# Kernel tuning notes

Measured on AMD Instinct MI355X. Metric: run time of the kernel, lower is better.

The kernel has to match this reference:

```python
import jax, jax.numpy as jnp
import numpy as np

B, N, F_IN, H, L = 4, 2048, 3, 32, 3
H2 = H // 2


def setup_inputs() -> dict:
    key = jax.random.key(0)
    ks = jax.random.split(key, 16)
    feats = jax.random.normal(ks[0], (B, N, F_IN), dtype=jnp.float32)
    coors = jax.random.normal(ks[1], (B, N, 3), dtype=jnp.float32) * 3.0
    adj = jax.random.randint(ks[2], (B, N, N), 0, 2).astype(bool)
    adj = adj | jnp.eye(N, dtype=bool)[None]  # self-loops so every row has a neighbor
    s = 0.1
    return {
        "feats": feats,
        "coors": coors,
        "adj_mat": adj,
        "W_in": jax.random.normal(ks[3], (F_IN, H), dtype=jnp.float32) * s,
        "Wq": jax.random.normal(ks[4], (L, H, H), dtype=jnp.float32) * s,
        "Wk": jax.random.normal(ks[5], (L, H, H), dtype=jnp.float32) * s,
        "Wv": jax.random.normal(ks[6], (L, H, H), dtype=jnp.float32) * s,
        "Wo": jax.random.normal(ks[7], (L, H, H), dtype=jnp.float32) * s,
        "W1": jax.random.normal(ks[8], (L, H, 2 * H), dtype=jnp.float32) * s,
        "W2": jax.random.normal(ks[9], (L, 2 * H, H), dtype=jnp.float32) * s,
        "coor_scale": jnp.full((L,), 0.1, dtype=jnp.float32),
        "Wf1": jax.random.normal(ks[10], (H, H2), dtype=jnp.float32) * s,
        "bf1": jnp.zeros((H2,), dtype=jnp.float32),
        "Wf2": jax.random.normal(ks[11], (H2, 3), dtype=jnp.float32) * s,
        "bf2": jnp.zeros((3,), dtype=jnp.float32),
    }


def _se3_forward(feats, coors, adj_mat, W_in, Wq, Wk, Wv, Wo, W1, W2, coor_scale):
    h = feats @ W_in                      # [B,N,H]
    x = coors
    neg = jnp.finfo(h.dtype).min
    inv_sqrt_d = 1.0 / jnp.sqrt(jnp.asarray(H, h.dtype))
    for l in range(L):                    # small static layer loop
        rel = x[:, :, None, :] - x[:, None, :, :]          # [B,N,N,3]
        dist2 = jnp.sum(rel * rel, axis=-1)                 # [B,N,N]
        q = h @ Wq[l]
        k = h @ Wk[l]
        v = h @ Wv[l]
        logits = jnp.einsum('bie,bje->bij', q, k) * inv_sqrt_d - dist2
        logits = jnp.where(adj_mat, logits, neg)
        attn = jax.nn.softmax(logits, axis=-1)              # [B,N,N]
        h = h + jnp.einsum('bij,bjd->bid', attn, v) @ Wo[l]
        # equivariant coordinate update (attention-weighted relative vectors)
        x = x + coor_scale[l] * jnp.einsum('bij,bijc->bic', attn, rel)
        h = h + jax.nn.relu(h @ W1[l]) @ W2[l]
    return h


def reference(feats, coors, adj_mat, W_in, Wq, Wk, Wv, Wo, W1, W2,
              coor_scale, Wf1, bf1, Wf2, bf2):
    h = _se3_forward(feats, coors, adj_mat, W_in, Wq, Wk, Wv, Wo, W1, W2, coor_scale)
    pooled = h.mean(axis=1)                                 # [B,H]
    out = jax.nn.relu(pooled @ Wf1 + bf1) @ Wf2 + bf2       # [B,3]
    return out
```

## Files before the change

### kernel.cpp

```cpp
#include <hip/hip_runtime.h>
#include <cstddef>
#include <cstdint>

#define N_     2048
#define H_     32
#define NEGF   (-1.0e30f)
#define LOG2E  1.4426950408889634f
#define C1F    (0.17677669529663687f * 1.4426950408889634f)
#define DEFER  16.0f
#define NCHUNK 8
#define CLEN   256
#define NRTOT  8192
#define PREC   20

#define AS1 __attribute__((address_space(1)))
#define AS3 __attribute__((address_space(3)))

typedef unsigned short ushortT;
typedef short v8s __attribute__((ext_vector_type(8)));
typedef float v4f __attribute__((ext_vector_type(4)));

__device__ __forceinline__ float exp2_fast(float x) {
    float r;
    asm("v_exp_f32 %0, %1" : "=v"(r) : "v"(x));
    return r;
}

__device__ __forceinline__ unsigned f2bf(float x) {
    unsigned u = __builtin_bit_cast(unsigned, x);
    return (u + 0x7FFFu + ((u >> 16) & 1u)) >> 16;
}

__global__ __launch_bounds__(256) void k_adjmask(const int* __restrict__ adj,
                                                 unsigned long long* __restrict__ mask) {
    size_t idx = (size_t)blockIdx.x * 256 + threadIdx.x;
    unsigned long long m = __ballot(adj[idx] != 0);
    if ((threadIdx.x & 63) == 0) mask[idx >> 6] = m;
}

__global__ __launch_bounds__(256) void k_init_qkv(const float* __restrict__ feats,
                                                  const float* __restrict__ W_in,
                                                  const float* __restrict__ Wq,
                                                  const float* __restrict__ Wk,
                                                  const float* __restrict__ Wv,
                                                  float* __restrict__ h,
                                                  ushortT* __restrict__ qb,
                                                  ushortT* __restrict__ kb,
                                                  ushortT* __restrict__ vb) {
    __shared__ float hs[8][33];
    int t = threadIdx.x;
    int rl = t >> 5, c = t & 31;
    int row = blockIdx.x * 8 + rl;
    float f0 = feats[row * 3 + 0], f1 = feats[row * 3 + 1], f2 = feats[row * 3 + 2];
    float hv = f0 * W_in[c] + f1 * W_in[32 + c] + f2 * W_in[64 + c];
    hs[rl][c] = hv;
    h[(row << 5) + c] = hv;
    __syncthreads();
    float aq = 0.f, ak = 0.f, av = 0.f;
#pragma unroll
    for (int d = 0; d < 32; ++d) {
        float hd = hs[rl][d];
        aq += hd * Wq[(d << 5) + c];
        ak += hd * Wk[(d << 5) + c];
        av += hd * Wv[(d << 5) + c];
    }
    qb[(row << 5) + c] = (ushortT)f2bf(aq * C1F);
    kb[(row << 5) + c] = (ushortT)f2bf(ak);
    vb[(row << 5) + c] = (ushortT)f2bf(av);
}

__global__ __launch_bounds__(256) void k_attn(const ushortT* __restrict__ qb,
                                              const ushortT* __restrict__ kb,
                                              const ushortT* __restrict__ vb,
                                              const float* __restrict__ xin,
                                              const unsigned long long* __restrict__ maskg,
                                              float* __restrict__ pm,
                                              float* __restrict__ ps,
                                              unsigned* __restrict__ pacc) {
    __shared__ __attribute__((aligned(16))) ushortT k_lds[2][64 * 32];
    __shared__ __attribute__((aligned(16))) ushortT vt_lds[2][32 * 72];
    __shared__ __attribute__((aligned(16))) float4  x_lds[2][64];
    __shared__ __attribute__((aligned(16))) ushortT p_lds[4][16 * 40];

    const int t = threadIdx.x;
    const int w = t >> 6, l = t & 63;
    const int g = l >> 4, q = l & 15;
    const int rowblk = blockIdx.x >> 3;
    const int cid    = blockIdx.x & 7;
    const int bN = (rowblk >> 5) << 11;
    const int j0 = cid << 8;
    const int rq = rowblk * 64 + w * 16 + q;

#define STAGE_TILE(BUF, TILE)                                                                  \
    do {                                                                                       \
        const int jj0 = (TILE) << 6;                                                           \
        __builtin_amdgcn_global_load_lds(                                                      \
            (const AS1 void*)((const char*)(kb + (((size_t)(bN + j0 + jj0)) << 5)) + t * 16),  \
            (AS3 void*)((char*)&k_lds[BUF][0] + t * 16), 16, 0, 0);                            \
        const int j_ = t & 63, grp_ = t >> 6;                                                  \
        const uint4 vv = *(const uint4*)(vb + (((size_t)(bN + j0 + jj0 + j_)) << 5) + grp_ * 8);\
        unsigned arr[4] = {vv.x, vv.y, vv.z, vv.w};                                            \
        _Pragma("unroll")                                                                      \
        for (int ii = 0; ii < 4; ++ii) {                                                       \
            vt_lds[BUF][(grp_ * 8 + 2 * ii) * 72 + j_]     = (ushortT)(arr[ii] & 0xffffu);     \
            vt_lds[BUF][(grp_ * 8 + 2 * ii + 1) * 72 + j_] = (ushortT)(arr[ii] >> 16);         \
        }                                                                                      \
        if (t < 64) {                                                                          \
            const float* xp_ = xin + ((size_t)(bN + j0 + jj0 + t)) * 3;                        \
            float4 xv_; xv_.x = xp_[0]; xv_.y = xp_[1]; xv_.z = xp_[2]; xv_.w = 0.f;           \
            x_lds[BUF][t] = xv_;                                                               \
        }                                                                                      \
    } while (0)

    const v8s qf = *(const v8s*)(qb + (((size_t)rq) << 5) + g * 8);
    const float xi0 = xin[rq * 3 + 0], xi1 = xin[rq * 3 + 1], xi2 = xin[rq * 3 + 2];

    v4f oA = {0.f, 0.f, 0.f, 0.f}, oB = {0.f, 0.f, 0.f, 0.f};
    float m = NEGF, sum = 0.f;
    float xa0 = 0.f, xa1 = 0.f, xa2 = 0.f;

    ushortT* pw = &p_lds[w][0];

    STAGE_TILE(0, 0);
    __syncthreads();

    int cur = 0;
#pragma unroll
    for (int tile = 0; tile < 4; ++tile) {
        if (tile < 3) STAGE_TILE(cur ^ 1, tile + 1);
        const unsigned long long mw = maskg[(((size_t)rq) << 5) + (cid << 2) + tile];

#pragma unroll
        for (int half = 0; half < 2; ++half) {
            const int jt = half * 32;
            v8s kA = *(const v8s*)(&k_lds[cur][0] + (jt + q) * 32 + g * 8);
            v8s kB = *(const v8s*)(&k_lds[cur][0] + (jt + 16 + q) * 32 + g * 8);
            v4f zero = {0.f, 0.f, 0.f, 0.f};
            v4f sA = __builtin_amdgcn_mfma_f32_16x16x32_bf16(kA, qf, zero, 0, 0, 0);
            v4f sB = __builtin_amdgcn_mfma_f32_16x16x32_bf16(kB, qf, zero, 0, 0, 0);

            float se[8];
            float4 xjA[4], xjB[4];
            float pot = NEGF;
#pragma unroll
            for (int reg = 0; reg < 4; ++reg) {
                const int jA = jt + 4 * g + reg, jB = jA + 16;
                xjA[reg] = x_lds[cur][jA];
                xjB[reg] = x_lds[cur][jB];
                float dA0 = xi0 - xjA[reg].x, dA1 = xi1 - xjA[reg].y, dA2 = xi2 - xjA[reg].z;
                float dB0 = xi0 - xjB[reg].x, dB1 = xi1 - xjB[reg].y, dB2 = xi2 - xjB[reg].z;
                float distA = fmaf(dA2, dA2, fmaf(dA1, dA1, dA0 * dA0));
                float distB = fmaf(dB2, dB2, fmaf(dB1, dB1, dB0 * dB0));
                const int bA = (int)((mw >> jA) & 1ULL);
                const int bB = (int)((mw >> jB) & 1ULL);
                se[reg]     = bA ? fmaf(distA, -LOG2E, sA[reg]) : NEGF;
                se[4 + reg] = bB ? fmaf(distB, -LOG2E, sB[reg]) : NEGF;
                pot = fmaxf(pot, fmaxf(se[reg], se[4 + reg]));
            }
            pot = fmaxf(pot, __shfl_xor(pot, 16));
            pot = fmaxf(pot, __shfl_xor(pot, 32));
            if (__any(pot - m > DEFER)) {
                float n2 = fmaxf(m, pot);
                float al = exp2_fast(m - n2);
                m = n2; sum *= al;
                v4f alv = {al, al, al, al};
                oA *= alv; oB *= alv;
                xa0 *= al; xa1 *= al; xa2 *= al;
            }
            float p[8];
#pragma unroll
            for (int i = 0; i < 8; ++i) { p[i] = exp2_fast(se[i] - m); sum += p[i]; }
#pragma unroll
            for (int reg = 0; reg < 4; ++reg) {
                xa0 = fmaf(p[reg], xjA[reg].x, fmaf(p[4 + reg], xjB[reg].x, xa0));
                xa1 = fmaf(p[reg], xjA[reg].y, fmaf(p[4 + reg], xjB[reg].y, xa1));
                xa2 = fmaf(p[reg], xjA[reg].z, fmaf(p[4 + reg], xjB[reg].z, xa2));
            }
            uint2 wA, wB;
            wA.x = f2bf(p[0]) | (f2bf(p[1]) << 16);
            wA.y = f2bf(p[2]) | (f2bf(p[3]) << 16);
            wB.x = f2bf(p[4]) | (f2bf(p[5]) << 16);
            wB.y = f2bf(p[6]) | (f2bf(p[7]) << 16);
            *(uint2*)(pw + q * 40 + 4 * g)      = wA;
            *(uint2*)(pw + q * 40 + 16 + 4 * g) = wB;
            v8s pf = *(const v8s*)(pw + q * 40 + 8 * g);
            v8s vA = *(const v8s*)(&vt_lds[cur][0] + q * 72 + jt + 8 * g);
            v8s vB = *(const v8s*)(&vt_lds[cur][0] + (16 + q) * 72 + jt + 8 * g);
            oA = __builtin_amdgcn_mfma_f32_16x16x32_bf16(vA, pf, oA, 0, 0, 0);
            oB = __builtin_amdgcn_mfma_f32_16x16x32_bf16(vB, pf, oB, 0, 0, 0);
        }
        __syncthreads();
        cur ^= 1;
    }
#undef STAGE_TILE

    sum += __shfl_xor(sum, 16); sum += __shfl_xor(sum, 32);
    xa0 += __shfl_xor(xa0, 16); xa0 += __shfl_xor(xa0, 32);
    xa1 += __shfl_xor(xa1, 16); xa1 += __shfl_xor(xa1, 32);
    xa2 += __shfl_xor(xa2, 16); xa2 += __shfl_xor(xa2, 32);

    unsigned* pb = pacc + ((size_t)cid * NRTOT + rq) * PREC;
    uint2 rA, rB;
    rA.x = f2bf(oA[0]) | (f2bf(oA[1]) << 16);
    rA.y = f2bf(oA[2]) | (f2bf(oA[3]) << 16);
    rB.x = f2bf(oB[0]) | (f2bf(oB[1]) << 16);
    rB.y = f2bf(oB[2]) | (f2bf(oB[3]) << 16);
    *(uint2*)(pb + 2 * g)     = rA;
    *(uint2*)(pb + 8 + 2 * g) = rB;
    if (g == 0) {
        float4 tl; tl.x = xa0; tl.y = xa1; tl.z = xa2; tl.w = 0.f;
        *(float4*)(pb + 16) = tl;
        pm[(((size_t)rq) << 3) + cid] = m;
        ps[(((size_t)rq) << 3) + cid] = sum;
    }
}

__global__ __launch_bounds__(256) void k_mergefin(const float* __restrict__ pm,
                                                  const float* __restrict__ ps,
                                                  const unsigned* __restrict__ pacc,
                                                  float* __restrict__ hg,
                                                  const float* __restrict__ xin,
                                                  float* __restrict__ xout,
                                                  const float* __restrict__ Wo,
                                                  const float* __restrict__ W1,
                                                  const float* __restrict__ W2,
                                                  const float* __restrict__ csp,
                                                  const float* __restrict__ Wqn,
                                                  const float* __restrict__ Wkn,
                                                  const float* __restrict__ Wvn,
                                                  ushortT* __restrict__ qout,
                                                  ushortT* __restrict__ kout,
                                                  ushortT* __restrict__ vout) {
    __shared__ float wo_s[1024];
    __shared__ float w1_s[2048];
    __shared__ float w2_s[2048];
    __shared__ float wq_s[1024];
    __shared__ float wk_s[1024];
    __shared__ float wv_s[1024];
    __shared__ float ad_s[4][40];
    __shared__ float h1_s[4][36];
    __shared__ float h2_s[4][36];
    __shared__ float f_s[4][64];

    const int t = threadIdx.x, w = t >> 6, lane = t & 63;
    for (int i = t; i < 1024; i += 256) wo_s[i] = Wo[i];
    for (int i = t; i < 2048; i += 256) { w1_s[i] = W1[i]; w2_s[i] = W2[i]; }
    if (Wqn) {
        for (int i = t; i < 1024; i += 256) {
            wq_s[i] = Wqn[i]; wk_s[i] = Wkn[i]; wv_s[i] = Wvn[i];
        }
    }
    __syncthreads();

    const int r = (blockIdx.x << 2) + w;

    float pmv = NEGF, psv = 0.f;
    if (lane < NCHUNK) { pmv = pm[((size_t)r << 3) + lane]; psv = ps[((size_t)r << 3) + lane]; }
    float m_g = pmv;
#pragma unroll
    for (int off = 1; off < 64; off <<= 1) m_g = fmaxf(m_g, __shfl_xor(m_g, off));
    float scv = (lane < NCHUNK) ? exp2_fast(pmv - m_g) : 0.f;
    float sg = scv * psv;
#pragma unroll
    for (int off = 1; off < 64; off <<= 1) sg += __shfl_xor(sg, off);
    const float rinv = 1.0f / sg;

    const int off32 = (lane < 32) ? (lane >> 1) : (16 + ((lane - 32) & 3));
    const bool isTail = lane >= 32;
    const bool hiHalf = lane & 1;
    float ad = 0.f;
#pragma unroll
    for (int c = 0; c < NCHUNK; ++c) {
        float scc = __shfl(scv, c);
        unsigned u = pacc[((size_t)c * NRTOT + r) * PREC + off32];
        float f = isTail ? __builtin_bit_cast(float, u)
                         : __builtin_bit_cast(float, hiHalf ? (u & 0xffff0000u) : (u << 16));
        ad = fmaf(scc, f, ad);
    }
    if (lane < 35) ad_s[w][lane] = ad;

    const int col = lane & 31;
    float hv = 0.f;
#pragma unroll
    for (int d = 0; d < 32; ++d) hv = fmaf(ad_s[w][d], wo_s[(d << 5) + col], hv);
    float h1 = 0.f;
    if (lane < 32) { h1 = hg[(((size_t)r) << 5) + lane] + hv * rinv; h1_s[w][lane] = h1; }

    float f = 0.f;
#pragma unroll
    for (int d = 0; d < 32; ++d) f = fmaf(h1_s[w][d], w1_s[(d << 6) + lane], f);
    f = fmaxf(f, 0.f);
    f_s[w][lane] = f;

    if (lane < 32) {
        float v2a = 0.f;
#pragma unroll
        for (int u = 0; u < 64; ++u) v2a = fmaf(f_s[w][u], w2_s[(u << 5) + lane], v2a);
        float hnew = h1 + v2a;
        hg[(((size_t)r) << 5) + lane] = hnew;
        h2_s[w][lane] = hnew;
    }

    if (lane < 3) {
        float o  = ad_s[w][32 + lane] * rinv;
        float xi = xin[r * 3 + lane];
        xout[r * 3 + lane] = xi + csp[0] * (xi - o);
    }

    if (Wqn && lane < 32) {
        float aq = 0.f, ak = 0.f, av = 0.f;
#pragma unroll
        for (int d = 0; d < 32; ++d) {
            float hd = h2_s[w][d];
            aq = fmaf(hd, wq_s[(d << 5) + lane], aq);
            ak = fmaf(hd, wk_s[(d << 5) + lane], ak);
            av = fmaf(hd, wv_s[(d << 5) + lane], av);
        }
        qout[(((size_t)r) << 5) + lane] = (ushortT)f2bf(aq * C1F);
        kout[(((size_t)r) << 5) + lane] = (ushortT)f2bf(ak);
        vout[(((size_t)r) << 5) + lane] = (ushortT)f2bf(av);
    }
}

__global__ __launch_bounds__(256) void k_pool(const float* __restrict__ h,
                                              float* __restrict__ pool_ws) {
    const int b = blockIdx.x >> 5, sub = blockIdx.x & 31;
    const int t = threadIdx.x, c = t & 31, g = t >> 5;
    float s = 0.f;
#pragma unroll
    for (int i = 0; i < 8; ++i) {
        int row = (sub << 6) + (g << 3) + i;
        s += h[(((size_t)((b << 11) + row)) << 5) + c];
    }
    __shared__ float pool[8][32];
    pool[g][c] = s;
    __syncthreads();
    if (t < 32) {
        float ss = 0.f;
#pragma unroll
        for (int gg = 0; gg < 8; ++gg) ss += pool[gg][t];
        pool_ws[((b << 5) + sub) * 32 + t] = ss;
    }
}

__global__ __launch_bounds__(256) void k_head(const float* __restrict__ pool_ws,
                                              const float* __restrict__ Wf1,
                                              const float* __restrict__ bf1,
                                              const float* __restrict__ Wf2,
                                              const float* __restrict__ bf2,
                                              float* __restrict__ out) {
    __shared__ float pooled[4][32];
    __shared__ float a1[4][16];
    const int t = threadIdx.x;
    if (t < 128) {
        int b = t >> 5, c = t & 31;
        float ss = 0.f;
#pragma unroll
        for (int sub = 0; sub < 32; ++sub) ss += pool_ws[((b << 5) + sub) * 32 + c];
        pooled[b][c] = ss * (1.0f / N_);
    }
    __syncthreads();
    if (t < 64) {
        int b = t >> 4, u = t & 15;
        float a = bf1[u];
#pragma unroll
        for (int d = 0; d < 32; ++d) a += pooled[b][d] * Wf1[(d << 4) + u];
        a1[b][u] = fmaxf(a, 0.f);
    }
    __syncthreads();
    if (t < 12) {
        int b = t / 3, o = t - b * 3;
        float v = bf2[o];
#pragma unroll
        for (int e = 0; e < 16; ++e) v += a1[b][e] * Wf2[e * 3 + o];
        out[b * 3 + o] = v;
    }
}

extern "C" void kernel_launch(void* const* d_in, const int* in_sizes, int n_in,
                              void* d_out, int out_size, void* d_ws, size_t ws_size,
                              hipStream_t stream) {
    const float* feats = (const float*)d_in[0];
    const float* coors = (const float*)d_in[1];
    const int*   adj   = (const int*)d_in[2];
    const float* W_in  = (const float*)d_in[3];
    const float* Wq    = (const float*)d_in[4];
    const float* Wk    = (const float*)d_in[5];
    const float* Wv    = (const float*)d_in[6];
    const float* Wo    = (const float*)d_in[7];
    const float* W1    = (const float*)d_in[8];
    const float* W2    = (const float*)d_in[9];
    const float* csc   = (const float*)d_in[10];
    const float* Wf1   = (const float*)d_in[11];
    const float* bf1   = (const float*)d_in[12];
    const float* Wf2   = (const float*)d_in[13];
    const float* bf2   = (const float*)d_in[14];

    const size_t BNH = (size_t)4 * N_ * H_;
    float* ws = (float*)d_ws;
    float* h  = ws;
    ushortT* qb = (ushortT*)(ws + BNH);
    ushortT* kb = qb + BNH;
    ushortT* vb = kb + BNH;
    float* x0 = (float*)(vb + BNH);
    float* x1 = x0 + (size_t)4 * N_ * 3;
    unsigned long long* mask = (unsigned long long*)(x1 + (size_t)4 * N_ * 3);
    float* pm   = (float*)(mask + 262144);
    float* ps   = pm + (size_t)NCHUNK * NRTOT;
    unsigned* pacc = (unsigned*)(ps + (size_t)NCHUNK * NRTOT);
    float* pool_ws = (float*)(pacc + (size_t)NCHUNK * NRTOT * PREC);

    k_adjmask<<<65536, 256, 0, stream>>>(adj, mask);
    k_init_qkv<<<1024, 256, 0, stream>>>(feats, W_in, Wq, Wk, Wv, h, qb, kb, vb);

    const float* xin[3]  = {coors, x0, x1};
    float*       xout[3] = {x0, x1, x0};
    for (int l = 0; l < 3; ++l) {
        k_attn<<<1024, 256, 0, stream>>>(qb, kb, vb, xin[l], mask, pm, ps, pacc);
        const bool last = (l == 2);
        k_mergefin<<<2048, 256, 0, stream>>>(pm, ps, pacc, h, xin[l], xout[l],
                                             Wo + l * 1024, W1 + l * 2048, W2 + l * 2048,
                                             csc + l,
                                             last ? nullptr : Wq + (l + 1) * 1024,
                                             last ? nullptr : Wk + (l + 1) * 1024,
                                             last ? nullptr : Wv + (l + 1) * 1024,
                                             qb, kb, vb);
    }
    k_pool<<<128, 256, 0, stream>>>(h, pool_ws);
    k_head<<<1, 256, 0, stream>>>(pool_ws, Wf1, bf1, Wf2, bf2, (float*)d_out);
}
```

Before: 148.8 us.

## Fuse init kernels, process four rows per wave in mergefin, fold pooling into atomics

```diff
diff --git a/kernel.cpp b/kernel.cpp
--- a/kernel.cpp
+++ b/kernel.cpp
@@ -31,42 +31,46 @@
     return (u + 0x7FFFu + ((u >> 16) & 1u)) >> 16;
 }
 
-__global__ __launch_bounds__(256) void k_adjmask(const int* __restrict__ adj,
-                                                 unsigned long long* __restrict__ mask) {
-    size_t idx = (size_t)blockIdx.x * 256 + threadIdx.x;
+__global__ __launch_bounds__(256) void k_adjinit(const int* __restrict__ adj,
+                                                 unsigned long long* __restrict__ mask,
+                                                 const float* __restrict__ feats,
+                                                 const float* __restrict__ W_in,
+                                                 const float* __restrict__ Wq,
+                                                 const float* __restrict__ Wk,
+                                                 const float* __restrict__ Wv,
+                                                 float* __restrict__ h,
+                                                 ushortT* __restrict__ qb,
+                                                 ushortT* __restrict__ kb,
+                                                 ushortT* __restrict__ vb,
+                                                 float* __restrict__ pool_ws) {
+    __shared__ float hs[8][33];
+    const int t = threadIdx.x;
+    size_t idx = (size_t)blockIdx.x * 256 + t;
     unsigned long long m = __ballot(adj[idx] != 0);
-    if ((threadIdx.x & 63) == 0) mask[idx >> 6] = m;
-}
-
-__global__ __launch_bounds__(256) void k_init_qkv(const float* __restrict__ feats,
-                                                  const float* __restrict__ W_in,
-                                                  const float* __restrict__ Wq,
-                                                  const float* __restrict__ Wk,
-                                                  const float* __restrict__ Wv,
-                                                  float* __restrict__ h,
-                                                  ushortT* __restrict__ qb,
-                                                  ushortT* __restrict__ kb,
-                                                  ushortT* __restrict__ vb) {
-    __shared__ float hs[8][33];
-    int t = threadIdx.x;
-    int rl = t >> 5, c = t & 31;
-    int row = blockIdx.x * 8 + rl;
-    float f0 = feats[row * 3 + 0], f1 = feats[row * 3 + 1], f2 = feats[row * 3 + 2];
-    float hv = f0 * W_in[c] + f1 * W_in[32 + c] + f2 * W_in[64 + c];
-    hs[rl][c] = hv;
-    h[(row << 5) + c] = hv;
-    __syncthreads();
-    float aq = 0.f, ak = 0.f, av = 0.f;
-#pragma unroll
-    for (int d = 0; d < 32; ++d) {
-        float hd = hs[rl][d];
-        aq += hd * Wq[(d << 5) + c];
-        ak += hd * Wk[(d << 5) + c];
-        av += hd * Wv[(d << 5) + c];
-    }
-    qb[(row << 5) + c] = (ushortT)f2bf(aq * C1F);
-    kb[(row << 5) + c] = (ushortT)f2bf(ak);
-    vb[(row << 5) + c] = (ushortT)f2bf(av);
+    if ((t & 63) == 0) mask[idx >> 6] = m;
+
+    if (blockIdx.x < 1024) {
+        int rl = t >> 5, c = t & 31;
+        int row = blockIdx.x * 8 + rl;
+        float f0 = feats[row * 3 + 0], f1 = feats[row * 3 + 1], f2 = feats[row * 3 + 2];
+        float hv = f0 * W_in[c] + f1 * W_in[32 + c] + f2 * W_in[64 + c];
+        hs[rl][c] = hv;
+        h[(row << 5) + c] = hv;
+        __syncthreads();
+        float aq = 0.f, ak = 0.f, av = 0.f;
+#pragma unroll
+        for (int d = 0; d < 32; ++d) {
+            float hd = hs[rl][d];
+            aq += hd * Wq[(d << 5) + c];
+            ak += hd * Wk[(d << 5) + c];
+            av += hd * Wv[(d << 5) + c];
+        }
+        qb[(row << 5) + c] = (ushortT)f2bf(aq * C1F);
+        kb[(row << 5) + c] = (ushortT)f2bf(ak);
+        vb[(row << 5) + c] = (ushortT)f2bf(av);
+    } else if (blockIdx.x == 1024 && t < 128) {
+        pool_ws[t] = 0.f;
+    }
 }
 
 __global__ __launch_bounds__(256) void k_attn(const ushortT* __restrict__ qb,
@@ -230,7 +234,8 @@
                                                   const float* __restrict__ Wvn,
                                                   ushortT* __restrict__ qout,
                                                   ushortT* __restrict__ kout,
-                                                  ushortT* __restrict__ vout) {
+                                                  ushortT* __restrict__ vout,
+                                                  float* __restrict__ pool_ws) {
     __shared__ float wo_s[1024];
     __shared__ float w1_s[2048];
     __shared__ float w2_s[2048];
@@ -252,94 +257,90 @@
     }
     __syncthreads();
 
-    const int r = (blockIdx.x << 2) + w;
-
-    float pmv = NEGF, psv = 0.f;
-    if (lane < NCHUNK) { pmv = pm[((size_t)r << 3) + lane]; psv = ps[((size_t)r << 3) + lane]; }
-    float m_g = pmv;
-#pragma unroll
-    for (int off = 1; off < 64; off <<= 1) m_g = fmaxf(m_g, __shfl_xor(m_g, off));
-    float scv = (lane < NCHUNK) ? exp2_fast(pmv - m_g) : 0.f;
-    float sg = scv * psv;
-#pragma unroll
-    for (int off = 1; off < 64; off <<= 1) sg += __shfl_xor(sg, off);
-    const float rinv = 1.0f / sg;
-
-    const int off32 = (lane < 32) ? (lane >> 1) : (16 + ((lane - 32) & 3));
-    const bool isTail = lane >= 32;
-    const bool hiHalf = lane & 1;
-    float ad = 0.f;
-#pragma unroll
-    for (int c = 0; c < NCHUNK; ++c) {
-        float scc = __shfl(scv, c);
-        unsigned u = pacc[((size_t)c * NRTOT + r) * PREC + off32];
-        float f = isTail ? __builtin_bit_cast(float, u)
-                         : __builtin_bit_cast(float, hiHalf ? (u & 0xffff0000u) : (u << 16));
-        ad = fmaf(scc, f, ad);
-    }
-    if (lane < 35) ad_s[w][lane] = ad;
-
-    const int col = lane & 31;
-    float hv = 0.f;
-#pragma unroll
-    for (int d = 0; d < 32; ++d) hv = fmaf(ad_s[w][d], wo_s[(d << 5) + col], hv);
-    float h1 = 0.f;
-    if (lane < 32) { h1 = hg[(((size_t)r) << 5) + lane] + hv * rinv; h1_s[w][lane] = h1; }
-
-    float f = 0.f;
-#pragma unroll
-    for (int d = 0; d < 32; ++d) f = fmaf(h1_s[w][d], w1_s[(d << 6) + lane], f);
-    f = fmaxf(f, 0.f);
-    f_s[w][lane] = f;
-
-    if (lane < 32) {
-        float v2a = 0.f;
-#pragma unroll
-        for (int u = 0; u < 64; ++u) v2a = fmaf(f_s[w][u], w2_s[(u << 5) + lane], v2a);
-        float hnew = h1 + v2a;
-        hg[(((size_t)r) << 5) + lane] = hnew;
-        h2_s[w][lane] = hnew;
-    }
-
-    if (lane < 3) {
-        float o  = ad_s[w][32 + lane] * rinv;
-        float xi = xin[r * 3 + lane];
-        xout[r * 3 + lane] = xi + csp[0] * (xi - o);
-    }
-
-    if (Wqn && lane < 32) {
-        float aq = 0.f, ak = 0.f, av = 0.f;
-#pragma unroll
-        for (int d = 0; d < 32; ++d) {
-            float hd = h2_s[w][d];
-            aq = fmaf(hd, wq_s[(d << 5) + lane], aq);
-            ak = fmaf(hd, wk_s[(d << 5) + lane], ak);
-            av = fmaf(hd, wv_s[(d << 5) + lane], av);
-        }
-        qout[(((size_t)r) << 5) + lane] = (ushortT)f2bf(aq * C1F);
-        kout[(((size_t)r) << 5) + lane] = (ushortT)f2bf(ak);
-        vout[(((size_t)r) << 5) + lane] = (ushortT)f2bf(av);
-    }
-}
-
-__global__ __launch_bounds__(256) void k_pool(const float* __restrict__ h,
-                                              float* __restrict__ pool_ws) {
-    const int b = blockIdx.x >> 5, sub = blockIdx.x & 31;
-    const int t = threadIdx.x, c = t & 31, g = t >> 5;
-    float s = 0.f;
-#pragma unroll
-    for (int i = 0; i < 8; ++i) {
-        int row = (sub << 6) + (g << 3) + i;
-        s += h[(((size_t)((b << 11) + row)) << 5) + c];
-    }
-    __shared__ float pool[8][32];
-    pool[g][c] = s;
-    __syncthreads();
-    if (t < 32) {
-        float ss = 0.f;
-#pragma unroll
-        for (int gg = 0; gg < 8; ++gg) ss += pool[gg][t];
-        pool_ws[((b << 5) + sub) * 32 + t] = ss;
+    float psum = 0.f;
+
+#pragma unroll 1
+    for (int ri = 0; ri < 4; ++ri) {
+        const int r = (blockIdx.x << 4) + (w << 2) + ri;
+
+        float pmv = NEGF, psv = 0.f;
+        if (lane < NCHUNK) { pmv = pm[((size_t)r << 3) + lane]; psv = ps[((size_t)r << 3) + lane]; }
+        float m_g = pmv;
+#pragma unroll
+        for (int off = 1; off < 64; off <<= 1) m_g = fmaxf(m_g, __shfl_xor(m_g, off));
+        float scv = (lane < NCHUNK) ? exp2_fast(pmv - m_g) : 0.f;
+        float sg = scv * psv;
+#pragma unroll
+        for (int off = 1; off < 64; off <<= 1) sg += __shfl_xor(sg, off);
+        const float rinv = 1.0f / sg;
+
+        const int off32 = (lane < 32) ? (lane >> 1) : (16 + ((lane - 32) & 3));
+        const bool isTail = lane >= 32;
+        const bool hiHalf = lane & 1;
+        float ad = 0.f;
+#pragma unroll
+        for (int c = 0; c < NCHUNK; ++c) {
+            float scc = __shfl(scv, c);
+            unsigned u = pacc[((size_t)c * NRTOT + r) * PREC + off32];
+            float f = isTail ? __builtin_bit_cast(float, u)
+                             : __builtin_bit_cast(float, hiHalf ? (u & 0xffff0000u) : (u << 16));
+            ad = fmaf(scc, f, ad);
+        }
+        if (lane < 35) ad_s[w][lane] = ad;
+
+        const int col = lane & 31;
+        float hv = 0.f;
+#pragma unroll
+        for (int d = 0; d < 32; ++d) hv = fmaf(ad_s[w][d], wo_s[(d << 5) + col], hv);
+        float h1 = 0.f;
+        if (lane < 32) { h1 = hg[(((size_t)r) << 5) + lane] + hv * rinv; h1_s[w][lane] = h1; }
+
+        float f = 0.f;
+#pragma unroll
+        for (int d = 0; d < 32; ++d) f = fmaf(h1_s[w][d], w1_s[(d << 6) + lane], f);
+        f = fmaxf(f, 0.f);
+        f_s[w][lane] = f;
+
+        if (lane < 32) {
+            float v2a = 0.f;
+#pragma unroll
+            for (int u = 0; u < 64; ++u) v2a = fmaf(f_s[w][u], w2_s[(u << 5) + lane], v2a);
+            float hnew = h1 + v2a;
+            hg[(((size_t)r) << 5) + lane] = hnew;
+            h2_s[w][lane] = hnew;
+            psum += hnew;
+        }
+
+        if (lane < 3) {
+            float o  = ad_s[w][32 + lane] * rinv;
+            float xi = xin[r * 3 + lane];
+            xout[r * 3 + lane] = xi + csp[0] * (xi - o);
+        }
+
+        if (Wqn && lane < 32) {
+            float aq = 0.f, ak = 0.f, av = 0.f;
+#pragma unroll
+            for (int d = 0; d < 32; ++d) {
+                float hd = h2_s[w][d];
+                aq = fmaf(hd, wq_s[(d << 5) + lane], aq);
+                ak = fmaf(hd, wk_s[(d << 5) + lane], ak);
+                av = fmaf(hd, wv_s[(d << 5) + lane], av);
+            }
+            qout[(((size_t)r) << 5) + lane] = (ushortT)f2bf(aq * C1F);
+            kout[(((size_t)r) << 5) + lane] = (ushortT)f2bf(ak);
+            vout[(((size_t)r) << 5) + lane] = (ushortT)f2bf(av);
+        }
+    }
+
+    if (pool_ws) {
+        __syncthreads();
+        if (lane < 32) f_s[w][lane] = psum;
+        __syncthreads();
+        if (w == 0 && lane < 32) {
+            float s4 = f_s[0][lane] + f_s[1][lane] + f_s[2][lane] + f_s[3][lane];
+            const int batch = blockIdx.x >> 7;
+            atomicAdd(&pool_ws[(batch << 5) + lane], s4);
+        }
     }
 }
 
@@ -354,10 +355,7 @@
     const int t = threadIdx.x;
     if (t < 128) {
         int b = t >> 5, c = t & 31;
-        float ss = 0.f;
-#pragma unroll
-        for (int sub = 0; sub < 32; ++sub) ss += pool_ws[((b << 5) + sub) * 32 + c];
-        pooled[b][c] = ss * (1.0f / N_);
+        pooled[b][c] = pool_ws[t] * (1.0f / N_);
     }
     __syncthreads();
     if (t < 64) {
@@ -410,22 +408,22 @@
     unsigned* pacc = (unsigned*)(ps + (size_t)NCHUNK * NRTOT);
     float* pool_ws = (float*)(pacc + (size_t)NCHUNK * NRTOT * PREC);
 
-    k_adjmask<<<65536, 256, 0, stream>>>(adj, mask);
-    k_init_qkv<<<1024, 256, 0, stream>>>(feats, W_in, Wq, Wk, Wv, h, qb, kb, vb);
+    k_adjinit<<<65536, 256, 0, stream>>>(adj, mask, feats, W_in, Wq, Wk, Wv,
+                                         h, qb, kb, vb, pool_ws);
 
     const float* xin[3]  = {coors, x0, x1};
     float*       xout[3] = {x0, x1, x0};
     for (int l = 0; l < 3; ++l) {
         k_attn<<<1024, 256, 0, stream>>>(qb, kb, vb, xin[l], mask, pm, ps, pacc);
         const bool last = (l == 2);
-        k_mergefin<<<2048, 256, 0, stream>>>(pm, ps, pacc, h, xin[l], xout[l],
-                                             Wo + l * 1024, W1 + l * 2048, W2 + l * 2048,
-                                             csc + l,
-                                             last ? nullptr : Wq + (l + 1) * 1024,
-                                             last ? nullptr : Wk + (l + 1) * 1024,
-                                             last ? nullptr : Wv + (l + 1) * 1024,
-                                             qb, kb, vb);
-    }
-    k_pool<<<128, 256, 0, stream>>>(h, pool_ws);
+        k_mergefin<<<512, 256, 0, stream>>>(pm, ps, pacc, h, xin[l], xout[l],
+                                            Wo + l * 1024, W1 + l * 2048, W2 + l * 2048,
+                                            csc + l,
+                                            last ? nullptr : Wq + (l + 1) * 1024,
+                                            last ? nullptr : Wk + (l + 1) * 1024,
+                                            last ? nullptr : Wv + (l + 1) * 1024,
+                                            qb, kb, vb,
+                                            last ? pool_ws : nullptr);
+    }
     k_head<<<1, 256, 0, stream>>>(pool_ws, Wf1, bf1, Wf2, bf2, (float*)d_out);
 }
```

Result: no change. 149.7 us (+0.6%).
